# Optimization experiments

Measured on AMD Instinct MI355X. Metric: run time of the kernel, lower is better.

The kernel has to match this reference:

```python
import jax, jax.numpy as jnp
import numpy as np
import math

B, S, V, D = 2, 2048, 32000, 256

def setup_inputs() -> dict:
    key = jax.random.key(0)
    ks = jax.random.split(key, 10)
    inp = jax.random.randint(ks[0], (B, S), 0, V)
    # causal mask, broadcast over batch
    mask = jnp.broadcast_to(jnp.tril(jnp.ones((S, S), dtype=bool)), (B, S, S))
    scale = 1.0 / math.sqrt(D)
    return {
        "input": inp,
        "mask": mask,
        "E": jax.random.normal(ks[1], (V, D), jnp.float32) * scale,
        "P": jax.random.normal(ks[2], (S, D), jnp.float32) * scale,
        "WQK1": jax.random.normal(ks[3], (D, D), jnp.float32) * scale,
        "WOV1": jax.random.normal(ks[4], (D, D), jnp.float32) * scale,
        "WQK2": jax.random.normal(ks[5], (D, D), jnp.float32) * scale,
        "WOV2": jax.random.normal(ks[6], (D, D), jnp.float32) * scale,
        "WF":   jax.random.normal(ks[7], (D, D), jnp.float32) * scale,
        "U":    jax.random.normal(ks[8], (V, D), jnp.float32) * scale,
    }

def _attn_block(X, WQK, WOV, mask, d_model):
    # S = (X @ WQK.T) @ X.T * sqrt(d)  -- note: MULTIPLY by sqrt(d), as in source
    scores = jnp.einsum('bsd,btd->bst', X @ WQK.T, X) * math.sqrt(d_model)
    scores = jnp.where(mask, scores, -jnp.inf)
    A = jax.nn.softmax(scores, axis=-1)  # dropout p=0 -> identity
    Y = jnp.einsum('bst,btd->bsd', A, X @ WOV.T)
    return X + Y

def reference(input, mask, E, P, WQK1, WOV1, WQK2, WOV2, WF, U):
    d_model = E.shape[1]
    X = E[input] + P[None, :, :]          # (B,S,D)
    X = _attn_block(X, WQK1, WOV1, mask, d_model)
    X = _attn_block(X, WQK2, WOV2, mask, d_model)
    X = X + X @ WF.T                      # FFN residual
    logits = X @ U.T                      # (B,S,V)
    return logits
```

## Files before the change

kernel.cpp:

```cpp
#include <hip/hip_runtime.h>
#include <math.h>

#define Bn 2
#define Sn 2048
#define Vn 32000
#define Dn 256
#define BSn (Bn * Sn)

typedef unsigned short u16;
typedef __attribute__((ext_vector_type(8))) __bf16 bf16x8;
typedef __attribute__((ext_vector_type(4))) float f32x4;
typedef __attribute__((ext_vector_type(8))) unsigned short u16x8;
typedef __attribute__((ext_vector_type(4))) unsigned short u16x4;

__device__ __forceinline__ u16 f2b(float v) {
    union { __bf16 b; u16 u; } c;
    c.b = (__bf16)v;
    return c.u;
}

#define GLOAD16(gp, lp)                                          \
    __builtin_amdgcn_global_load_lds(                            \
        (const __attribute__((address_space(1))) void*)(gp),     \
        (__attribute__((address_space(3))) void*)(lp), 16, 0, 0)

__device__ __forceinline__ float wred_max(float v) {
#pragma unroll
    for (int o = 32; o; o >>= 1) v = fmaxf(v, __shfl_xor(v, o, 64));
    return v;
}
__device__ __forceinline__ float wred_sum(float v) {
#pragma unroll
    for (int o = 32; o; o >>= 1) v += __shfl_xor(v, o, 64);
    return v;
}

__global__ __launch_bounds__(256) void k_prep(
    const int* __restrict__ inp, const float* __restrict__ E,
    const float* __restrict__ P, const float* __restrict__ WQK1,
    const float* __restrict__ WOV1, const float* __restrict__ WQK2,
    const float* __restrict__ WOV2, const float* __restrict__ WF,
    const float* __restrict__ U, float* __restrict__ Xf, u16* __restrict__ Xb,
    u16* __restrict__ Wqv1, u16* __restrict__ Wqv2, u16* __restrict__ Wfb,
    u16* __restrict__ Ub) {
    int bid = blockIdx.x;
    if (bid < 320) {
        int w = bid >> 6, blk = bid & 63;
        const float* src;
        u16* dst;
        switch (w) {
            case 0: src = WQK1; dst = Wqv1; break;
            case 1: src = WOV1; dst = Wqv1 + Dn * Dn; break;
            case 2: src = WQK2; dst = Wqv2; break;
            case 3: src = WOV2; dst = Wqv2 + Dn * Dn; break;
            default: src = WF; dst = Wfb; break;
        }
        int i = (blk * 256 + threadIdx.x) * 4;
        float4 v = *(const float4*)&src[i];
        u16x4 o;
        o.x = f2b(v.x); o.y = f2b(v.y); o.z = f2b(v.z); o.w = f2b(v.w);
        *(u16x4*)&dst[i] = o;
    } else if (bid < 8320) {
        int i = ((bid - 320) * 256 + threadIdx.x) * 4;
        float4 v = *(const float4*)&U[i];
        u16x4 o;
        o.x = f2b(v.x); o.y = f2b(v.y); o.z = f2b(v.z); o.w = f2b(v.w);
        *(u16x4*)&Ub[i] = o;
    } else {
        int bs = bid - 8320;
        int d = threadIdx.x;
        int tok = inp[bs];
        int s = bs & (Sn - 1);
        float v = E[(size_t)tok * Dn + d] + P[(size_t)s * Dn + d];
        Xf[(size_t)bs * Dn + d] = v;
        Xb[(size_t)bs * Dn + d] = f2b(v);
    }
}

template <bool HAS_RES, bool OUT_F32, bool OUT_BF16, bool CAUSAL_SKIP,
          bool QV_SPLIT, int CHUNK, int TN>
__global__ __launch_bounds__(256)
void k_mfma(const u16* __restrict__ A, const u16* __restrict__ Bb,
            const float* __restrict__ R, float* __restrict__ Cf,
            u16* __restrict__ Cb, u16* __restrict__ Ct, int M, int N, int K,
            int lda, int ldb, int ldc, float alpha, long long sA, long long sB,
            long long sC, long long sR, int ytiles) {
    int bx, by;
    if (CHUNK > 0) {
        int nwg = gridDim.x;
        int q = nwg >> 3;
        int bid = blockIdx.x;
        int wg = (bid & 7) * q + (bid >> 3);
        int per = CHUNK * ytiles;
        int ch = wg / per, rr = wg % per;
        bx = ch * CHUNK + rr % CHUNK;
        by = rr / CHUNK;
    } else {
        bx = blockIdx.x;
        by = blockIdx.y;
    }
    int bm0 = by * 128;
    int bn0 = bx * TN;
    if (CAUSAL_SKIP && bn0 > bm0 + 127) return;

    int zb = blockIdx.z;
    A += (long long)zb * sA;
    Bb += (long long)zb * sB;
    if (HAS_RES) R += (long long)zb * sR;
    if (OUT_F32) Cf += (long long)zb * sC;
    if (OUT_BF16) Cb += (long long)zb * sC;

    __shared__ alignas(16) u16 As[2][128 * 32];
    __shared__ alignas(16) u16 Bs[2][TN * 32];

    int tid = threadIdx.x;
    int lane = tid & 63;
    int wave = tid >> 6;

    constexpr int MF = (TN == 128) ? 4 : 2;
    int wr, wc;
    if (TN == 128) {
        wr = wave >> 1;
        wc = wave & 1;
    } else {
        wr = wave;
        wc = 0;
    }

    int fr = lane & 15;
    int kq = lane >> 4;
    int rq = kq * 4;

    f32x4 acc[MF][4] = {};

    int nt = K >> 5;

    auto STAGE = [&](int buf, int k0) {
#pragma unroll
        for (int c = 0; c < 2; ++c) {
            int idx = tid + c * 256;
            int r = idx >> 2, co = (idx & 3) << 3;
            GLOAD16(&A[(size_t)(bm0 + r) * lda + k0 + co], &As[buf][idx * 8]);
        }
#pragma unroll
        for (int c = 0; c < TN / 64; ++c) {
            int idx = tid + c * 256;
            int r = idx >> 2, co = (idx & 3) << 3;
            GLOAD16(&Bb[(size_t)(bn0 + r) * ldb + k0 + co], &Bs[buf][idx * 8]);
        }
    };

    STAGE(0, 0);
    __syncthreads();

    for (int t = 0; t < nt; ++t) {
        int cur = t & 1;
        if (t + 1 < nt) STAGE(cur ^ 1, (t + 1) << 5);

        bf16x8 a[MF], b[4];
#pragma unroll
        for (int m = 0; m < MF; ++m)
            a[m] = *(const bf16x8*)&As[cur]
                       [(wr * (MF * 16) + m * 16 + fr) * 32 + kq * 8];
#pragma unroll
        for (int n = 0; n < 4; ++n)
            b[n] = *(const bf16x8*)&Bs[cur]
                       [(wc * 64 + n * 16 + fr) * 32 + kq * 8];
#pragma unroll
        for (int m = 0; m < MF; ++m)
#pragma unroll
            for (int n = 0; n < 4; ++n)
                acc[m][n] = __builtin_amdgcn_mfma_f32_16x16x32_bf16(
                    a[m], b[n], acc[m][n], 0, 0, 0);
        __syncthreads();
    }

    if (QV_SPLIT && bn0 >= 256) {
#pragma unroll
        for (int m = 0; m < MF; ++m) {
#pragma unroll
            for (int n = 0; n < 4; ++n) {
                int gr = bm0 + wr * (MF * 16) + m * 16 + rq;
                int gc = bn0 + wc * 64 + n * 16 + fr - 256;
                int bb = gr / Sn;
                int ss = gr % Sn;
                u16x4 o;
#pragma unroll
                for (int i = 0; i < 4; ++i) o[i] = f2b(acc[m][n][i]);
                *(u16x4*)&Ct[((size_t)bb * Dn + gc) * Sn + ss] = o;
            }
        }
        return;
    }

#pragma unroll
    for (int m = 0; m < MF; ++m) {
#pragma unroll
        for (int n = 0; n < 4; ++n) {
            int gr = bm0 + wr * (MF * 16) + m * 16 + rq;
            int gc = bn0 + wc * 64 + n * 16 + fr;
#pragma unroll
            for (int i = 0; i < 4; ++i) {
                float v = acc[m][n][i] * alpha;
                size_t idx = (size_t)(gr + i) * ldc + gc;
                if (HAS_RES) v += R[idx];
                if (OUT_F32) Cf[idx] = v;
                if (OUT_BF16) Cb[idx] = f2b(v);
            }
        }
    }
}

__global__ __launch_bounds__(256)
void k_pv(const u16* __restrict__ Pb, const u16* __restrict__ Vt,
          const float* __restrict__ R, float* __restrict__ Cf,
          u16* __restrict__ Cb) {
    int bm0 = blockIdx.y * 64;
    int bn0 = blockIdx.x * 64;
    int zb = blockIdx.z;
    const u16* A = Pb + (long long)zb * Sn * Sn;
    const u16* Bb = Vt + (long long)zb * (long long)Dn * Sn;
    const float* Rz = R + (long long)zb * Sn * Dn;
    float* Cfz = Cf + (long long)zb * Sn * Dn;
    u16* Cbz = Cb + (long long)zb * Sn * Dn;

    __shared__ alignas(16) u16 As[3][64 * 32];
    __shared__ alignas(16) u16 Bs[3][64 * 32];

    int tid = threadIdx.x;
    int lane = tid & 63, wave = tid >> 6;
    int wr = wave >> 1, wc = wave & 1;
    int fr = lane & 15, kq = lane >> 4, rq = kq * 4;

    int nt = (bm0 + 64) >> 5;

    auto RSTAGE = [&](int buf, int t) {
        int k0 = t << 5;
        int r = tid >> 2, co = (tid & 3) << 3;
        GLOAD16(&A[(size_t)(bm0 + r) * Sn + k0 + co], &As[buf][tid * 8]);
        GLOAD16(&Bb[(size_t)(bn0 + r) * Sn + k0 + co], &Bs[buf][tid * 8]);
    };

    f32x4 acc[2][2] = {};
    RSTAGE(0, 0);
    RSTAGE(1, 1);

    for (int t = 0; t < nt; ++t) {
        if (t + 1 < nt)
            asm volatile("s_waitcnt vmcnt(2)" ::: "memory");
        else
            asm volatile("s_waitcnt vmcnt(0)" ::: "memory");
        __builtin_amdgcn_s_barrier();
        __builtin_amdgcn_sched_barrier(0);
        if (t + 2 < nt) RSTAGE((t + 2) % 3, t + 2);

        int cur = t % 3;
        bf16x8 a[2], b[2];
#pragma unroll
        for (int m = 0; m < 2; ++m)
            a[m] = *(const bf16x8*)&As[cur]
                       [(wr * 32 + m * 16 + fr) * 32 + kq * 8];
#pragma unroll
        for (int n = 0; n < 2; ++n)
            b[n] = *(const bf16x8*)&Bs[cur]
                       [(wc * 32 + n * 16 + fr) * 32 + kq * 8];
#pragma unroll
        for (int m = 0; m < 2; ++m)
#pragma unroll
            for (int n = 0; n < 2; ++n)
                acc[m][n] = __builtin_amdgcn_mfma_f32_16x16x32_bf16(
                    a[m], b[n], acc[m][n], 0, 0, 0);
    }

#pragma unroll
    for (int m = 0; m < 2; ++m) {
#pragma unroll
        for (int n = 0; n < 2; ++n) {
            int gr = bm0 + wr * 32 + m * 16 + rq;
            int gc = bn0 + wc * 32 + n * 16 + fr;
#pragma unroll
            for (int i = 0; i < 4; ++i) {
                float v = acc[m][n][i];
                size_t idx = (size_t)(gr + i) * Dn + gc;
                v += Rz[idx];
                Cfz[idx] = v;
                Cbz[idx] = f2b(v);
            }
        }
    }
}

__global__ __launch_bounds__(256) void k_softmax(const float* __restrict__ Sc,
                                                 u16* __restrict__ Pb) {
    int bs = blockIdx.x;
    int b = bs >> 11, s = bs & 2047;
    const float* row = Sc + ((size_t)b << 22) + ((size_t)s << 11);
    u16* prow = Pb + ((size_t)b << 22) + ((size_t)s << 11);
    int tid = threadIdx.x;
    int n = s + 1;
    int nc = (n + 127) & ~127;

    float v[8];
#pragma unroll
    for (int j = 0; j < 8; ++j) {
        int t = tid + j * 256;
        v[j] = (t < n) ? row[t] : -INFINITY;
    }

    float m = v[0];
#pragma unroll
    for (int j = 1; j < 8; ++j) m = fmaxf(m, v[j]);
    m = wred_max(m);

    __shared__ float red[8];
    int lane = tid & 63, w = tid >> 6;
    if (lane == 0) red[w] = m;
    __syncthreads();
    m = fmaxf(fmaxf(red[0], red[1]), fmaxf(red[2], red[3]));

    float sum = 0.0f;
#pragma unroll
    for (int j = 0; j < 8; ++j) {
        v[j] = __expf(v[j] - m);
        sum += v[j];
    }
    sum = wred_sum(sum);
    if (lane == 0) red[4 + w] = sum;
    __syncthreads();
    float inv = 1.0f / (red[4] + red[5] + red[6] + red[7]);

#pragma unroll
    for (int j = 0; j < 8; ++j) {
        int t = tid + j * 256;
        if (t < nc) prow[t] = f2b(v[j] * inv);
    }
}

static void launch_layer(const float* XfIn, float* XfOut, u16* Xb,
                         const u16* Wqv, u16* Qb, u16* Vt, float* Sc, u16* Pb,
                         hipStream_t stream) {
    k_mfma<false, false, true, false, true, 0, 64>
        <<<dim3(8, 32, 1), 256, 0, stream>>>(
            Xb, Wqv, nullptr, nullptr, Qb, Vt, BSn, 512, Dn, Dn, Dn, Dn, 1.0f,
            0, 0, 0, 0, 0);
    k_mfma<false, true, false, true, false, 0, 128>
        <<<dim3(Sn / 128, Sn / 128, Bn), 256, 0, stream>>>(
            Qb, Xb, nullptr, Sc, nullptr, nullptr, Sn, Sn, Dn, Dn, Dn, Sn,
            16.0f, (long long)Sn * Dn, (long long)Sn * Dn, (long long)Sn * Sn,
            0, 0);
    k_softmax<<<Bn * Sn, 256, 0, stream>>>(Sc, Pb);
    k_pv<<<dim3(Dn / 64, Sn / 64, Bn), 256, 0, stream>>>(Pb, Vt, XfIn, XfOut,
                                                         Xb);
}

extern "C" void kernel_launch(void* const* d_in, const int* in_sizes, int n_in,
                              void* d_out, int out_size, void* d_ws,
                              size_t ws_size, hipStream_t stream) {
    const int* inp = (const int*)d_in[0];
    const float* E = (const float*)d_in[2];
    const float* P = (const float*)d_in[3];
    const float* WQK1 = (const float*)d_in[4];
    const float* WOV1 = (const float*)d_in[5];
    const float* WQK2 = (const float*)d_in[6];
    const float* WOV2 = (const float*)d_in[7];
    const float* WF = (const float*)d_in[8];
    const float* U = (const float*)d_in[9];
    float* out = (float*)d_out;

    char* p = (char*)d_ws;
    auto alloc = [&](size_t bytes) {
        void* r = (void*)p;
        p += (bytes + 255) & ~(size_t)255;
        return r;
    };

    float* XfA = (float*)alloc((size_t)BSn * Dn * 4);
    float* XfB = (float*)alloc((size_t)BSn * Dn * 4);
    float* Sc = (float*)alloc((size_t)Bn * Sn * Sn * 4);
    u16* Xb = (u16*)alloc((size_t)BSn * Dn * 2);
    u16* Qb = (u16*)alloc((size_t)BSn * Dn * 2);
    u16* Vt = (u16*)alloc((size_t)Bn * Dn * Sn * 2);
    u16* Fb = (u16*)alloc((size_t)BSn * Dn * 2);
    u16* Pb = (u16*)alloc((size_t)Bn * Sn * Sn * 2);
    u16* Wqv1 = (u16*)alloc((size_t)512 * Dn * 2);
    u16* Wqv2 = (u16*)alloc((size_t)512 * Dn * 2);
    u16* Wfb = (u16*)alloc((size_t)Dn * Dn * 2);
    u16* Ub = (u16*)alloc((size_t)Vn * Dn * 2);

    k_prep<<<12416, 256, 0, stream>>>(inp, E, P, WQK1, WOV1, WQK2, WOV2, WF, U,
                                      XfA, Xb, Wqv1, Wqv2, Wfb, Ub);

    launch_layer(XfA, XfB, Xb, Wqv1, Qb, Vt, Sc, Pb, stream);
    launch_layer(XfB, XfA, Xb, Wqv2, Qb, Vt, Sc, Pb, stream);

    k_mfma<true, false, true, false, false, 0, 64>
        <<<dim3(4, 32, 1), 256, 0, stream>>>(
            Xb, Wfb, XfA, nullptr, Fb, nullptr, BSn, Dn, Dn, Dn, Dn, Dn, 1.0f,
            0, 0, 0, 0, 0);

    k_mfma<false, true, false, false, false, 25, 128>
        <<<dim3((Vn / 128) * (BSn / 128), 1, 1), 256, 0, stream>>>(
            Fb, Ub, nullptr, out, nullptr, nullptr, BSn, Vn, Dn, Dn, Dn, Vn,
            1.0f, 0, 0, 0, 0, BSn / 128);
}
```

Baseline: 262.8 us.

## Fuse U fp32-to-bf16 conversion into the logits GEMM loads

Drops the separate pass in the prep kernel that converted the 32000x256 unembedding matrix to bf16. A dedicated logits kernel now reads U as fp32 into registers, converts it, and writes it to LDS with double buffering. This removes a full read-write round trip of U, but each of the 32 row tiles now rereads fp32 U, doubling its bytes per tile. The kernel also spends extra VALU work and registers on the conversion inside the main loop.

```diff
diff --git a/kernel.cpp b/kernel.cpp
--- a/kernel.cpp
+++ b/kernel.cpp
@@ -40,9 +40,8 @@
     const float* __restrict__ P, const float* __restrict__ WQK1,
     const float* __restrict__ WOV1, const float* __restrict__ WQK2,
     const float* __restrict__ WOV2, const float* __restrict__ WF,
-    const float* __restrict__ U, float* __restrict__ Xf, u16* __restrict__ Xb,
-    u16* __restrict__ Wqv1, u16* __restrict__ Wqv2, u16* __restrict__ Wfb,
-    u16* __restrict__ Ub) {
+    float* __restrict__ Xf, u16* __restrict__ Xb, u16* __restrict__ Wqv1,
+    u16* __restrict__ Wqv2, u16* __restrict__ Wfb) {
     int bid = blockIdx.x;
     if (bid < 320) {
         int w = bid >> 6, blk = bid & 63;
@@ -60,14 +59,8 @@
         u16x4 o;
         o.x = f2b(v.x); o.y = f2b(v.y); o.z = f2b(v.z); o.w = f2b(v.w);
         *(u16x4*)&dst[i] = o;
-    } else if (bid < 8320) {
-        int i = ((bid - 320) * 256 + threadIdx.x) * 4;
-        float4 v = *(const float4*)&U[i];
-        u16x4 o;
-        o.x = f2b(v.x); o.y = f2b(v.y); o.z = f2b(v.z); o.w = f2b(v.w);
-        *(u16x4*)&Ub[i] = o;
     } else {
-        int bs = bid - 8320;
+        int bs = bid - 320;
         int d = threadIdx.x;
         int tok = inp[bs];
         int s = bs & (Sn - 1);
@@ -78,27 +71,14 @@
 }
 
 template <bool HAS_RES, bool OUT_F32, bool OUT_BF16, bool CAUSAL_SKIP,
-          bool QV_SPLIT, int CHUNK, int TN>
+          bool QV_SPLIT, int TN>
 __global__ __launch_bounds__(256)
 void k_mfma(const u16* __restrict__ A, const u16* __restrict__ Bb,
             const float* __restrict__ R, float* __restrict__ Cf,
             u16* __restrict__ Cb, u16* __restrict__ Ct, int M, int N, int K,
             int lda, int ldb, int ldc, float alpha, long long sA, long long sB,
-            long long sC, long long sR, int ytiles) {
-    int bx, by;
-    if (CHUNK > 0) {
-        int nwg = gridDim.x;
-        int q = nwg >> 3;
-        int bid = blockIdx.x;
-        int wg = (bid & 7) * q + (bid >> 3);
-        int per = CHUNK * ytiles;
-        int ch = wg / per, rr = wg % per;
-        bx = ch * CHUNK + rr % CHUNK;
-        by = rr / CHUNK;
-    } else {
-        bx = blockIdx.x;
-        by = blockIdx.y;
-    }
+            long long sC, long long sR) {
+    int bx = blockIdx.x, by = blockIdx.y;
     int bm0 = by * 128;
     int bn0 = bx * TN;
     if (CAUSAL_SKIP && bn0 > bm0 + 127) return;
@@ -207,6 +187,110 @@
                 if (OUT_F32) Cf[idx] = v;
                 if (OUT_BF16) Cb[idx] = f2b(v);
             }
+        }
+    }
+}
+
+template <int CHUNK>
+__global__ __launch_bounds__(256)
+void k_logits(const u16* __restrict__ A, const float* __restrict__ Uf,
+              float* __restrict__ Cf, int ytiles) {
+    constexpr int K = 256;
+    int nwg = gridDim.x;
+    int q = nwg >> 3;
+    int bid = blockIdx.x;
+    int wg = (bid & 7) * q + (bid >> 3);
+    int per = CHUNK * ytiles;
+    int ch = wg / per, rr = wg % per;
+    int bx = ch * CHUNK + rr % CHUNK;
+    int by = rr / CHUNK;
+    int bm0 = by * 128;
+    int bn0 = bx * 128;
+
+    __shared__ alignas(16) u16 As[2][128 * 32];
+    __shared__ alignas(16) u16 Bs[2][128 * 32];
+
+    int tid = threadIdx.x;
+    int lane = tid & 63;
+    int wave = tid >> 6;
+    int wr = wave >> 1, wc = wave & 1;
+    int fr = lane & 15, kq = lane >> 4, rq = kq * 4;
+
+    f32x4 acc[4][4] = {};
+
+    auto STAGE_A = [&](int buf, int k0) {
+#pragma unroll
+        for (int c = 0; c < 2; ++c) {
+            int idx = tid + c * 256;
+            int r = idx >> 2, co = (idx & 3) << 3;
+            GLOAD16(&A[(size_t)(bm0 + r) * K + k0 + co], &As[buf][idx * 8]);
+        }
+    };
+
+    float vv[2][8];
+    auto LOAD_B = [&](int k0) {
+#pragma unroll
+        for (int c = 0; c < 2; ++c) {
+            int idx = tid + c * 256;
+            int r = idx >> 2, co = (idx & 3) << 3;
+            const float* src = &Uf[(size_t)(bn0 + r) * K + k0 + co];
+            float4 v0 = *(const float4*)src;
+            float4 v1 = *(const float4*)(src + 4);
+            vv[c][0] = v0.x; vv[c][1] = v0.y; vv[c][2] = v0.z; vv[c][3] = v0.w;
+            vv[c][4] = v1.x; vv[c][5] = v1.y; vv[c][6] = v1.z; vv[c][7] = v1.w;
+        }
+    };
+    auto WRITE_B = [&](int buf) {
+#pragma unroll
+        for (int c = 0; c < 2; ++c) {
+            int idx = tid + c * 256;
+            u16x8 o;
+#pragma unroll
+            for (int e = 0; e < 8; ++e) o[e] = f2b(vv[c][e]);
+            *(u16x8*)&Bs[buf][idx * 8] = o;
+        }
+    };
+
+    LOAD_B(0);
+    WRITE_B(0);
+    STAGE_A(0, 0);
+    __syncthreads();
+
+    for (int t = 0; t < 8; ++t) {
+        int cur = t & 1;
+        bool pre = (t + 1 < 8);
+        if (pre) {
+            LOAD_B((t + 1) << 5);
+            STAGE_A(cur ^ 1, (t + 1) << 5);
+        }
+
+        bf16x8 a[4], b[4];
+#pragma unroll
+        for (int m = 0; m < 4; ++m)
+            a[m] = *(const bf16x8*)&As[cur][(wr * 64 + m * 16 + fr) * 32 + kq * 8];
+#pragma unroll
+        for (int n = 0; n < 4; ++n)
+            b[n] = *(const bf16x8*)&Bs[cur][(wc * 64 + n * 16 + fr) * 32 + kq * 8];
+#pragma unroll
+        for (int m = 0; m < 4; ++m)
+#pragma unroll
+            for (int n = 0; n < 4; ++n)
+                acc[m][n] = __builtin_amdgcn_mfma_f32_16x16x32_bf16(
+                    a[m], b[n], acc[m][n], 0, 0, 0);
+
+        if (pre) WRITE_B(cur ^ 1);
+        __syncthreads();
+    }
+
+#pragma unroll
+    for (int m = 0; m < 4; ++m) {
+#pragma unroll
+        for (int n = 0; n < 4; ++n) {
+            int gr = bm0 + wr * 64 + m * 16 + rq;
+            int gc = bn0 + wc * 64 + n * 16 + fr;
+#pragma unroll
+            for (int i = 0; i < 4; ++i)
+                Cf[(size_t)(gr + i) * Vn + gc] = acc[m][n][i];
         }
     }
 }
@@ -339,15 +423,15 @@
 static void launch_layer(const float* XfIn, float* XfOut, u16* Xb,
                          const u16* Wqv, u16* Qb, u16* Vt, float* Sc, u16* Pb,
                          hipStream_t stream) {
-    k_mfma<false, false, true, false, true, 0, 64>
+    k_mfma<false, false, true, false, true, 64>
         <<<dim3(8, 32, 1), 256, 0, stream>>>(
             Xb, Wqv, nullptr, nullptr, Qb, Vt, BSn, 512, Dn, Dn, Dn, Dn, 1.0f,
-            0, 0, 0, 0, 0);
-    k_mfma<false, true, false, true, false, 0, 128>
+            0, 0, 0, 0);
+    k_mfma<false, true, false, true, false, 128>
         <<<dim3(Sn / 128, Sn / 128, Bn), 256, 0, stream>>>(
             Qb, Xb, nullptr, Sc, nullptr, nullptr, Sn, Sn, Dn, Dn, Dn, Sn,
             16.0f, (long long)Sn * Dn, (long long)Sn * Dn, (long long)Sn * Sn,
-            0, 0);
+            0);
     k_softmax<<<Bn * Sn, 256, 0, stream>>>(Sc, Pb);
     k_pv<<<dim3(Dn / 64, Sn / 64, Bn), 256, 0, stream>>>(Pb, Vt, XfIn, XfOut,
                                                          Xb);
@@ -385,21 +469,18 @@
     u16* Wqv1 = (u16*)alloc((size_t)512 * Dn * 2);
     u16* Wqv2 = (u16*)alloc((size_t)512 * Dn * 2);
     u16* Wfb = (u16*)alloc((size_t)Dn * Dn * 2);
-    u16* Ub = (u16*)alloc((size_t)Vn * Dn * 2);
-
-    k_prep<<<12416, 256, 0, stream>>>(inp, E, P, WQK1, WOV1, WQK2, WOV2, WF, U,
-                                      XfA, Xb, Wqv1, Wqv2, Wfb, Ub);
+
+    k_prep<<<4416, 256, 0, stream>>>(inp, E, P, WQK1, WOV1, WQK2, WOV2, WF,
+                                     XfA, Xb, Wqv1, Wqv2, Wfb);
 
     launch_layer(XfA, XfB, Xb, Wqv1, Qb, Vt, Sc, Pb, stream);
     launch_layer(XfB, XfA, Xb, Wqv2, Qb, Vt, Sc, Pb, stream);
 
-    k_mfma<true, false, true, false, false, 0, 64>
+    k_mfma<true, false, true, false, false, 64>
         <<<dim3(4, 32, 1), 256, 0, stream>>>(
             Xb, Wfb, XfA, nullptr, Fb, nullptr, BSn, Dn, Dn, Dn, Dn, Dn, 1.0f,
-            0, 0, 0, 0, 0);
-
-    k_mfma<false, true, false, false, false, 25, 128>
-        <<<dim3((Vn / 128) * (BSn / 128), 1, 1), 256, 0, stream>>>(
-            Fb, Ub, nullptr, out, nullptr, nullptr, BSn, Vn, Dn, Dn, Dn, Vn,
-            1.0f, 0, 0, 0, 0, BSn / 128);
-}
+            0, 0, 0, 0);
+
+    k_logits<25><<<dim3((Vn / 128) * (BSn / 128), 1, 1), 256, 0, stream>>>(
+        Fb, U, out, BSn / 128);
+}
```

Result: slower. 282.7 us (+7.6%).
